# Performance work log

Measured on AMD Instinct MI355X. Metric: run time of the kernel, lower is better.

## Reference

```python
import jax, jax.numpy as jnp
import numpy as np


def chamfer_l2(x, y):
    # x: [B,N1,3], y: [B,N2,3]; squared-L2 pairwise distances via Gram trick
    x2 = jnp.sum(x * x, axis=-1)                     # [B,N1]
    y2 = jnp.sum(y * y, axis=-1)                     # [B,N2]
    xy = jnp.einsum('bnd,bmd->bnm', x, y)            # [B,N1,N2]
    d = x2[:, :, None] + y2[:, None, :] - 2.0 * xy   # [B,N1,N2]
    cham_x = jnp.min(d, axis=2)                      # [B,N1] min over gt
    cham_y = jnp.min(d, axis=1)                      # [B,N2] min over pred
    return jnp.mean(cham_x) + jnp.mean(cham_y)


def setup_inputs() -> dict:
    key = jax.random.key(0)
    k1, k2, k3 = jax.random.split(key, 3)
    B = 4
    coarse_pc = jax.random.normal(k1, (B, 1024, 3), dtype=jnp.float32)
    fine_pc = jax.random.normal(k2, (B, 8192, 3), dtype=jnp.float32)
    gt_pc = jax.random.normal(k3, (B, 8192, 3), dtype=jnp.float32)
    return {"coarse_pc": coarse_pc, "fine_pc": fine_pc, "gt_pc": gt_pc,
            "param_coarse": 1000, "param_fine": 1000}


def reference(coarse_pc, fine_pc, gt_pc, param_coarse, param_fine):
    loss_coarse = chamfer_l2(coarse_pc, gt_pc) * param_coarse
    loss_fine = chamfer_l2(fine_pc, gt_pc) * param_fine
    return jnp.stack([loss_coarse, loss_fine])
```

## Files before the change

kernel.cpp:

```cpp
#include <hip/hip_runtime.h>

constexpr int NMINS = 102400;
constexpr int NBLK  = 1152;

typedef __attribute__((ext_vector_type(8)))  short bf16x8;
typedef __attribute__((ext_vector_type(16))) float f32x16;


__global__ __launch_bounds__(256) void pccl_stage(
    const float* __restrict__ Xc, const float* __restrict__ Xf,
    const float* __restrict__ G, unsigned* __restrict__ mins)
{
    __shared__ uint4 ysh[1024];
    const int tid  = threadIdx.x;
    const int lane = tid & 63;
    const int wv   = __builtin_amdgcn_readfirstlane(tid >> 6);
    const int W    = blockIdx.x;

    const float* Xp; const float* Yp;
    int NX, NY, ls, lc, local, mbase;
    if (W < 64)        { Xp=Xc; Yp=G;  NX=1024; NY=8192; ls=3; lc=1; local=W;     mbase=0; }
    else if (W < 128)  { Xp=G;  Yp=Xc; NX=8192; NY=1024; ls=0; lc=4; local=W-64;  mbase=4096; }
    else if (W < 640)  { Xp=Xf; Yp=G;  NX=8192; NY=8192; ls=3; lc=4; local=W-128; mbase=36864; }
    else               { Xp=G;  Yp=Xf; NX=8192; NY=8192; ls=3; lc=4; local=W-640; mbase=69632; }
    const int split  = local & ((1 << ls) - 1);
    const int rest   = local >> ls;
    const int chunk4 = rest & ((1 << lc) - 1);
    const int b      = rest >> lc;

    const float* yg = Yp + ((size_t)b * NY + (size_t)split * 1024) * 3;
    #pragma unroll
    for (int it = 0; it < 4; ++it) {
        const int pt = tid + 256 * it;
        const float y0 = yg[pt*3+0], y1 = yg[pt*3+1], y2 = yg[pt*3+2];
        const unsigned uh0 = __float_as_uint(y0) & 0xFFFF0000u;
        const unsigned uh1 = __float_as_uint(y1) & 0xFFFF0000u;
        const unsigned uh2 = __float_as_uint(y2) & 0xFFFF0000u;
        const unsigned sl0 = __float_as_uint(y0 - __uint_as_float(uh0)) >> 16;
        const unsigned sl1 = __float_as_uint(y1 - __uint_as_float(uh1)) >> 16;
        const unsigned sl2 = __float_as_uint(y2 - __uint_as_float(uh2)) >> 16;
        const float w = fmaf(y0, y0, fmaf(y1, y1, y2 * y2));
        const unsigned uhw = __float_as_uint(w) & 0xFFFF0000u;
        const unsigned slw = __float_as_uint(w - __uint_as_float(uhw)) >> 16;
        ysh[pt] = make_uint4((uh0>>16)|(sl0<<16), (uh1>>16)|(sl1<<16),
                             (uh2>>16)|(sl2<<16), (uhw>>16)|(slw<<16));
    }

    const int l31 = lane & 31;
    const bool hi = (lane >> 5) != 0;
    const float* xg = Xp + ((size_t)b * NX + (size_t)chunk4 * 512 + (size_t)wv * 128) * 3;
    bf16x8 Bf[4];
    float x2s[4];
    #pragma unroll
    for (int f = 0; f < 4; ++f) {
        const int p = f * 32 + l31;
        const float x0 = xg[p*3+0], x1 = xg[p*3+1], x2 = xg[p*3+2];
        x2s[f] = fmaf(x0, x0, fmaf(x1, x1, x2 * x2));
        const float m0 = -2.f * x0, m1 = -2.f * x1, m2 = -2.f * x2;
        const unsigned uh0 = __float_as_uint(m0) & 0xFFFF0000u;
        const unsigned uh1 = __float_as_uint(m1) & 0xFFFF0000u;
        const unsigned uh2 = __float_as_uint(m2) & 0xFFFF0000u;
        const unsigned sh0 = uh0 >> 16, sh1 = uh1 >> 16, sh2 = uh2 >> 16;
        const unsigned sl0 = __float_as_uint(m0 - __uint_as_float(uh0)) >> 16;
        const unsigned sl1 = __float_as_uint(m1 - __uint_as_float(uh1)) >> 16;
        const unsigned sl2 = __float_as_uint(m2 - __uint_as_float(uh2)) >> 16;
        union { unsigned u[4]; bf16x8 v; } bu;
        bu.u[0] = hi ? (sl2 | (0x3F80u << 16)) : (sh0 | (sh0 << 16));
        bu.u[1] = hi ? 0x3F80u                 : (sl0 | (sh1 << 16));
        bu.u[2] = hi ? 0u                      : (sh1 | (sl1 << 16));
        bu.u[3] = hi ? 0u                      : (sh2 | (sh2 << 16));
        Bf[f] = bu.v;
    }

    __syncthreads();

    float best[4][8];
    #pragma unroll
    for (int f = 0; f < 4; ++f)
        #pragma unroll
        for (int j = 0; j < 8; ++j) best[f][j] = 3.0e38f;

    const f32x16 zc = (f32x16)0.0f;

    #pragma unroll 2
    for (int t = 0; t < 32; ++t) {
        const uint4 dd = ysh[t * 32 + l31];
        union { unsigned u[4]; bf16x8 v; } au;
        au.u[0] = hi ? ((dd.z & 0xFFFFu) | (dd.w << 16))
                     : dd.x;
        au.u[1] = hi ? (dd.w >> 16)
                     : ((dd.x & 0xFFFFu) | (dd.y << 16));
        au.u[2] = hi ? 0u : ((dd.y >> 16) | (dd.y << 16));
        au.u[3] = hi ? 0u : dd.z;
        const bf16x8 Af = au.v;
        #pragma unroll
        for (int f = 0; f < 4; ++f) {
            const f32x16 acc = __builtin_amdgcn_mfma_f32_32x32x16_bf16(Af, Bf[f], zc, 0, 0, 0);
            #pragma unroll
            for (int j = 0; j < 8; ++j)
                best[f][j] = fminf(fminf(best[f][j], acc[2*j]), acc[2*j+1]);
        }
    }

    unsigned* mp = mins + mbase + b * NX + chunk4 * 512 + wv * 128;
    #pragma unroll
    for (int f = 0; f < 4; ++f) {
        const float m0 = fminf(fminf(best[f][0], best[f][1]), best[f][2]);
        const float m1 = fminf(fminf(best[f][3], best[f][4]), best[f][5]);
        const float m2 = fminf(fminf(best[f][6], best[f][7]), m0);
        float tm = fminf(m1, m2);
        tm = fminf(tm, __shfl_xor(tm, 32, 64));
        const float d = fmaxf(x2s[f] + tm, 0.0f);
        atomicMin(mp + f * 32 + l31, __float_as_uint(d));
    }
}

__global__ __launch_bounds__(256) void pccl_sum(
    const unsigned* __restrict__ mins,
    const int* __restrict__ pc, const int* __restrict__ pf,
    float* __restrict__ out)
{
    const int tid = blockIdx.x * 256 + threadIdx.x;
    const uint4 v = ((const uint4*)mins)[tid];
    float s = __uint_as_float(v.x) + __uint_as_float(v.y)
            + __uint_as_float(v.z) + __uint_as_float(v.w);
    #pragma unroll
    for (int off = 32; off > 0; off >>= 1) s += __shfl_down(s, off, 64);
    if ((threadIdx.x & 63) == 0) {
        const int i = tid * 4;
        float scale, param; int o;
        if (i < 4096)       { scale = 1.f / 4096.f;  param = (float)pc[0]; o = 0; }
        else if (i < 36864) { scale = 1.f / 32768.f; param = (float)pc[0]; o = 0; }
        else                { scale = 1.f / 32768.f; param = (float)pf[0]; o = 1; }
        atomicAdd(out + o, s * scale * param);
    }
}

extern "C" void kernel_launch(void* const* d_in, const int* in_sizes, int n_in,
                              void* d_out, int out_size, void* d_ws, size_t ws_size,
                              hipStream_t stream) {
    const float* coarse = (const float*)d_in[0];
    const float* fine   = (const float*)d_in[1];
    const float* gt     = (const float*)d_in[2];
    const int*   pc     = (const int*)d_in[3];
    const int*   pf     = (const int*)d_in[4];
    float* out = (float*)d_out;
    unsigned* mins = (unsigned*)d_ws;

    hipMemsetAsync(mins, 0x7F, (size_t)NMINS * 4, stream);
    hipMemsetAsync(out, 0, 2 * sizeof(float), stream);
    pccl_stage<<<NBLK, 256, 0, stream>>>(coarse, fine, gt, mins);
    pccl_sum<<<NMINS / 1024, 256, 0, stream>>>(mins, pc, pf, out);
}
```

Measured before the change: 100.4 us.

## Loop each block over all Y chunks, drop atomicMin buffer and memsets

Each block now loops over every 1024-point Y chunk internally instead of splitting Y across blocks. This removes the global atomicMin scratch array, both memsets, and the big reduction kernel; blocks write one partial sum each and a single-block kernel finishes. The LDS layout is pre-split into separate lo/hi uint4 arrays so the MFMA A operand loads directly without per-iteration select/shift work. Dropping from 1152 to 200 blocks on a 256-CU device risks underfilling the GPU and lengthens each block's serial loop, which now includes repeated staging syncs.

Result: slower. 146.8 us (+46.2%).

```diff
diff --git a/kernel.cpp b/kernel.cpp
--- a/kernel.cpp
+++ b/kernel.cpp
@@ -1,69 +1,47 @@
 #include <hip/hip_runtime.h>
 
-constexpr int NMINS = 102400;
-constexpr int NBLK  = 1152;
+constexpr int NSTAGE = 200;
 
 typedef __attribute__((ext_vector_type(8)))  short bf16x8;
 typedef __attribute__((ext_vector_type(16))) float f32x16;
 
+__device__ __forceinline__ void split2(float v, unsigned& h, unsigned& l) {
+    const unsigned uh = __float_as_uint(v) & 0xFFFF0000u;
+    h = uh >> 16;
+    l = __float_as_uint(v - __uint_as_float(uh)) >> 16;
+}
 
 __global__ __launch_bounds__(256) void pccl_stage(
     const float* __restrict__ Xc, const float* __restrict__ Xf,
-    const float* __restrict__ G, unsigned* __restrict__ mins)
+    const float* __restrict__ G, float* __restrict__ partials)
 {
-    __shared__ uint4 ysh[1024];
+    __shared__ uint4 alo[1024];
+    __shared__ uint4 ahi[1024];
+    __shared__ float psh[4];
     const int tid  = threadIdx.x;
     const int lane = tid & 63;
     const int wv   = __builtin_amdgcn_readfirstlane(tid >> 6);
+    const int l31  = lane & 31;
+    const bool hi  = lane >= 32;
     const int W    = blockIdx.x;
 
-    const float* Xp; const float* Yp;
-    int NX, NY, ls, lc, local, mbase;
-    if (W < 64)        { Xp=Xc; Yp=G;  NX=1024; NY=8192; ls=3; lc=1; local=W;     mbase=0; }
-    else if (W < 128)  { Xp=G;  Yp=Xc; NX=8192; NY=1024; ls=0; lc=4; local=W-64;  mbase=4096; }
-    else if (W < 640)  { Xp=Xf; Yp=G;  NX=8192; NY=8192; ls=3; lc=4; local=W-128; mbase=36864; }
-    else               { Xp=G;  Yp=Xf; NX=8192; NY=8192; ls=3; lc=4; local=W-640; mbase=69632; }
-    const int split  = local & ((1 << ls) - 1);
-    const int rest   = local >> ls;
-    const int chunk4 = rest & ((1 << lc) - 1);
-    const int b      = rest >> lc;
+    const float* Xp; const float* Yp; int NX, NY, b, chunk;
+    if (W < 8)        {              Xp=Xc; Yp=G;  NX=1024; NY=8192; b=W>>1; chunk=W&1; }
+    else if (W < 72)  { int l=W-8;   Xp=G;  Yp=Xc; NX=8192; NY=1024; b=l>>4; chunk=l&15; }
+    else if (W < 136) { int l=W-72;  Xp=Xf; Yp=G;  NX=8192; NY=8192; b=l>>4; chunk=l&15; }
+    else              { int l=W-136; Xp=G;  Yp=Xf; NX=8192; NY=8192; b=l>>4; chunk=l&15; }
 
-    const float* yg = Yp + ((size_t)b * NY + (size_t)split * 1024) * 3;
-    #pragma unroll
-    for (int it = 0; it < 4; ++it) {
-        const int pt = tid + 256 * it;
-        const float y0 = yg[pt*3+0], y1 = yg[pt*3+1], y2 = yg[pt*3+2];
-        const unsigned uh0 = __float_as_uint(y0) & 0xFFFF0000u;
-        const unsigned uh1 = __float_as_uint(y1) & 0xFFFF0000u;
-        const unsigned uh2 = __float_as_uint(y2) & 0xFFFF0000u;
-        const unsigned sl0 = __float_as_uint(y0 - __uint_as_float(uh0)) >> 16;
-        const unsigned sl1 = __float_as_uint(y1 - __uint_as_float(uh1)) >> 16;
-        const unsigned sl2 = __float_as_uint(y2 - __uint_as_float(uh2)) >> 16;
-        const float w = fmaf(y0, y0, fmaf(y1, y1, y2 * y2));
-        const unsigned uhw = __float_as_uint(w) & 0xFFFF0000u;
-        const unsigned slw = __float_as_uint(w - __uint_as_float(uhw)) >> 16;
-        ysh[pt] = make_uint4((uh0>>16)|(sl0<<16), (uh1>>16)|(sl1<<16),
-                             (uh2>>16)|(sl2<<16), (uhw>>16)|(slw<<16));
-    }
-
-    const int l31 = lane & 31;
-    const bool hi = (lane >> 5) != 0;
-    const float* xg = Xp + ((size_t)b * NX + (size_t)chunk4 * 512 + (size_t)wv * 128) * 3;
-    bf16x8 Bf[4];
-    float x2s[4];
+    const float* xg = Xp + ((size_t)b * NX + (size_t)chunk * 512 + (size_t)wv * 128) * 3;
+    bf16x8 Bf[4]; float x2s[4];
     #pragma unroll
     for (int f = 0; f < 4; ++f) {
         const int p = f * 32 + l31;
         const float x0 = xg[p*3+0], x1 = xg[p*3+1], x2 = xg[p*3+2];
         x2s[f] = fmaf(x0, x0, fmaf(x1, x1, x2 * x2));
-        const float m0 = -2.f * x0, m1 = -2.f * x1, m2 = -2.f * x2;
-        const unsigned uh0 = __float_as_uint(m0) & 0xFFFF0000u;
-        const unsigned uh1 = __float_as_uint(m1) & 0xFFFF0000u;
-        const unsigned uh2 = __float_as_uint(m2) & 0xFFFF0000u;
-        const unsigned sh0 = uh0 >> 16, sh1 = uh1 >> 16, sh2 = uh2 >> 16;
-        const unsigned sl0 = __float_as_uint(m0 - __uint_as_float(uh0)) >> 16;
-        const unsigned sl1 = __float_as_uint(m1 - __uint_as_float(uh1)) >> 16;
-        const unsigned sl2 = __float_as_uint(m2 - __uint_as_float(uh2)) >> 16;
+        unsigned sh0, sl0, sh1, sl1, sh2, sl2;
+        split2(-2.f * x0, sh0, sl0);
+        split2(-2.f * x1, sh1, sl1);
+        split2(-2.f * x2, sh2, sl2);
         union { unsigned u[4]; bf16x8 v; } bu;
         bu.u[0] = hi ? (sl2 | (0x3F80u << 16)) : (sh0 | (sh0 << 16));
         bu.u[1] = hi ? 0x3F80u                 : (sl0 | (sh1 << 16));
@@ -72,8 +50,6 @@
         Bf[f] = bu.v;
     }
 
-    __syncthreads();
-
     float best[4][8];
     #pragma unroll
     for (int f = 0; f < 4; ++f)
@@ -81,28 +57,41 @@
         for (int j = 0; j < 8; ++j) best[f][j] = 3.0e38f;
 
     const f32x16 zc = (f32x16)0.0f;
+    const uint4* __restrict__ abase = hi ? ahi : alo;
 
-    #pragma unroll 2
-    for (int t = 0; t < 32; ++t) {
-        const uint4 dd = ysh[t * 32 + l31];
-        union { unsigned u[4]; bf16x8 v; } au;
-        au.u[0] = hi ? ((dd.z & 0xFFFFu) | (dd.w << 16))
-                     : dd.x;
-        au.u[1] = hi ? (dd.w >> 16)
-                     : ((dd.x & 0xFFFFu) | (dd.y << 16));
-        au.u[2] = hi ? 0u : ((dd.y >> 16) | (dd.y << 16));
-        au.u[3] = hi ? 0u : dd.z;
-        const bf16x8 Af = au.v;
+    for (int c = 0; c < NY / 1024; ++c) {
+        __syncthreads();
+        const float* yg = Yp + ((size_t)b * NY + (size_t)c * 1024) * 3;
         #pragma unroll
-        for (int f = 0; f < 4; ++f) {
-            const f32x16 acc = __builtin_amdgcn_mfma_f32_32x32x16_bf16(Af, Bf[f], zc, 0, 0, 0);
+        for (int it = 0; it < 4; ++it) {
+            const int pt = tid + 256 * it;
+            const float y0 = yg[pt*3+0], y1 = yg[pt*3+1], y2 = yg[pt*3+2];
+            const float w  = fmaf(y0, y0, fmaf(y1, y1, y2 * y2));
+            unsigned h0, L0, h1, L1, h2, L2, hw, Lw;
+            split2(y0, h0, L0); split2(y1, h1, L1);
+            split2(y2, h2, L2); split2(w,  hw, Lw);
+            alo[pt] = make_uint4(h0 | (L0 << 16), h0 | (h1 << 16),
+                                 L1 | (h1 << 16), h2 | (L2 << 16));
+            ahi[pt] = make_uint4(h2 | (hw << 16), Lw, 0u, 0u);
+        }
+        __syncthreads();
+
+        #pragma unroll 4
+        for (int t = 0; t < 32; ++t) {
+            const uint4 dd = abase[t * 32 + l31];
+            union { uint4 u; bf16x8 v; } au; au.u = dd;
+            const bf16x8 Af = au.v;
             #pragma unroll
-            for (int j = 0; j < 8; ++j)
-                best[f][j] = fminf(fminf(best[f][j], acc[2*j]), acc[2*j+1]);
+            for (int f = 0; f < 4; ++f) {
+                const f32x16 acc = __builtin_amdgcn_mfma_f32_32x32x16_bf16(Af, Bf[f], zc, 0, 0, 0);
+                #pragma unroll
+                for (int j = 0; j < 8; ++j)
+                    best[f][j] = fminf(fminf(best[f][j], acc[2*j]), acc[2*j+1]);
+            }
         }
     }
 
-    unsigned* mp = mins + mbase + b * NX + chunk4 * 512 + wv * 128;
+    float s = 0.f;
     #pragma unroll
     for (int f = 0; f < 4; ++f) {
         const float m0 = fminf(fminf(best[f][0], best[f][1]), best[f][2]);
@@ -110,29 +99,37 @@
         const float m2 = fminf(fminf(best[f][6], best[f][7]), m0);
         float tm = fminf(m1, m2);
         tm = fminf(tm, __shfl_xor(tm, 32, 64));
-        const float d = fmaxf(x2s[f] + tm, 0.0f);
-        atomicMin(mp + f * 32 + l31, __float_as_uint(d));
+        s += fmaxf(x2s[f] + tm, 0.0f);
     }
+    #pragma unroll
+    for (int off = 1; off < 64; off <<= 1) s += __shfl_xor(s, off, 64);
+    if (lane == 0) psh[wv] = s * 0.5f;
+    __syncthreads();
+    if (tid == 0) partials[W] = psh[0] + psh[1] + psh[2] + psh[3];
 }
 
 __global__ __launch_bounds__(256) void pccl_sum(
-    const unsigned* __restrict__ mins,
+    const float* __restrict__ partials,
     const int* __restrict__ pc, const int* __restrict__ pf,
     float* __restrict__ out)
 {
-    const int tid = blockIdx.x * 256 + threadIdx.x;
-    const uint4 v = ((const uint4*)mins)[tid];
-    float s = __uint_as_float(v.x) + __uint_as_float(v.y)
-            + __uint_as_float(v.z) + __uint_as_float(v.w);
+    const int tid = threadIdx.x;
+    const int lane = tid & 63;
+    const int wv = tid >> 6;
+    float v = (tid < NSTAGE) ? partials[tid] : 0.f;
+    float w0 = (tid < 8) ? v * (1.f/4096.f) : ((tid < 72) ? v * (1.f/32768.f) : 0.f);
+    float w1 = (tid >= 72) ? v * (1.f/32768.f) : 0.f;
     #pragma unroll
-    for (int off = 32; off > 0; off >>= 1) s += __shfl_down(s, off, 64);
-    if ((threadIdx.x & 63) == 0) {
-        const int i = tid * 4;
-        float scale, param; int o;
-        if (i < 4096)       { scale = 1.f / 4096.f;  param = (float)pc[0]; o = 0; }
-        else if (i < 36864) { scale = 1.f / 32768.f; param = (float)pc[0]; o = 0; }
-        else                { scale = 1.f / 32768.f; param = (float)pf[0]; o = 1; }
-        atomicAdd(out + o, s * scale * param);
+    for (int off = 1; off < 64; off <<= 1) {
+        w0 += __shfl_xor(w0, off, 64);
+        w1 += __shfl_xor(w1, off, 64);
+    }
+    __shared__ float s0[4], s1[4];
+    if (lane == 0) { s0[wv] = w0; s1[wv] = w1; }
+    __syncthreads();
+    if (tid == 0) {
+        out[0] = (s0[0] + s0[1] + s0[2] + s0[3]) * (float)pc[0];
+        out[1] = (s1[0] + s1[1] + s1[2] + s1[3]) * (float)pf[0];
     }
 }
 
@@ -145,10 +142,8 @@
     const int*   pc     = (const int*)d_in[3];
     const int*   pf     = (const int*)d_in[4];
     float* out = (float*)d_out;
-    unsigned* mins = (unsigned*)d_ws;
+    float* partials = (float*)d_ws;
 
-    hipMemsetAsync(mins, 0x7F, (size_t)NMINS * 4, stream);
-    hipMemsetAsync(out, 0, 2 * sizeof(float), stream);
-    pccl_stage<<<NBLK, 256, 0, stream>>>(coarse, fine, gt, mins);
-    pccl_sum<<<NMINS / 1024, 256, 0, stream>>>(mins, pc, pf, out);
+    pccl_stage<<<NSTAGE, 256, 0, stream>>>(coarse, fine, gt, partials);
+    pccl_sum<<<1, 256, 0, stream>>>(partials, pc, pf, out);
 }
```
